# Kernel tuning notes

Hardware: AMD Instinct MI355X
Metric: run time of the kernel (lower is better)

The kernel has to match this reference:

```python
import jax, jax.numpy as jnp
import numpy as np

B, N, NSAMPLE = 8, 2048, 32
D = 64          # input feature channels
C1, C2 = 64, 128  # MLP channels (channels list after +3 on input: 67 -> 64 -> 128)
RADIUS = 0.15
EPS = 1e-5


def setup_inputs() -> dict:
    key = jax.random.key(0)
    ks = jax.random.split(key, 4)
    position = jax.random.uniform(ks[0], (B, N, 3), dtype=jnp.float32)
    feature = jax.random.normal(ks[1], (B, N, D), dtype=jnp.float32)
    W1 = jax.random.normal(ks[2], (D + 3, C1), dtype=jnp.float32) * 0.05
    gamma1 = jnp.ones((C1,), jnp.float32)
    beta1 = jnp.zeros((C1,), jnp.float32)
    W2 = jax.random.normal(ks[3], (C1, C2), dtype=jnp.float32) * 0.05
    gamma2 = jnp.ones((C2,), jnp.float32)
    beta2 = jnp.zeros((C2,), jnp.float32)
    return {"position": position, "feature": feature,
            "W1": W1, "gamma1": gamma1, "beta1": beta1,
            "W2": W2, "gamma2": gamma2, "beta2": beta2}


def _ball_query(xyz, radius, nsample):
    # squared pairwise distances [B, N, N]
    sq = (jnp.sum(xyz ** 2, -1)[:, :, None]
          + jnp.sum(xyz ** 2, -1)[:, None, :]
          - 2.0 * jnp.einsum('bnc,bmc->bnm', xyz, xyz))
    n = xyz.shape[1]
    idx = jnp.where(sq > radius ** 2, n, jnp.arange(n, dtype=jnp.int32)[None, None, :])
    idx = jnp.sort(idx, axis=-1)[:, :, :nsample]            # [B, N, nsample]
    first = idx[:, :, :1]
    return jnp.where(idx == n, first, idx)                  # pad misses with first neighbor


def _gather(points, idx):
    # points [B, N, C], idx [B, S, K] -> [B, S, K, C]
    b, s, k = idx.shape
    flat = jnp.take_along_axis(points, idx.reshape(b, s * k, 1), axis=1)
    return flat.reshape(b, s, k, points.shape[-1])


def _bn_relu(x, gamma, beta, relu=True):
    # BatchNorm1d over channel dim (train-mode stats across B*N*S), per linearblock
    mean = jnp.mean(x, axis=(0, 1, 2), keepdims=True)
    var = jnp.var(x, axis=(0, 1, 2), keepdims=True)
    y = (x - mean) * jax.lax.rsqrt(var + EPS) * gamma + beta
    return jax.nn.relu(y) if relu else y


def reference(position, feature, W1, gamma1, beta1, W2, gamma2, beta2):
    b, n, _ = position.shape
    idx = _ball_query(position, RADIUS, NSAMPLE)            # [B, N, nsample]
    grouped_xyz = _gather(position, idx) - position[:, :, None, :]  # [B,N,ns,3]
    grouped_feat = _gather(feature, idx)                    # [B, N, ns, D]
    h = jnp.concatenate([grouped_xyz, grouped_feat], axis=-1)  # [B, N, ns, 3+D]
    h = _bn_relu(h @ W1, gamma1, beta1)                     # [B, N, ns, C1]
    h = _bn_relu(h @ W2, gamma2, beta2)                     # [B, N, ns, C2]
    new_feature = jnp.max(h, axis=2)                        # [B, N, C2]
    return position, new_feature
```

## Files before the change

kernel.cpp:

```cpp
#include <hip/hip_runtime.h>
#include <hip/hip_bf16.h>


#define BB 8
#define NN 2048
#define KK 32
#define DD 64
#define CC1 64
#define CC2 128
#define TOTROWS (BB*NN*KK)
#define SITES (BB*NN)
#define PSLICES 256
#define DBLOCKS 1024

typedef __bf16 bf16x8 __attribute__((ext_vector_type(8)));
typedef float  f32x4  __attribute__((ext_vector_type(4)));

__device__ __forceinline__ void lds_add(float* p, float v) {
  __hip_atomic_fetch_add(p, v, __ATOMIC_RELAXED, __HIP_MEMORY_SCOPE_WORKGROUP);
}

__global__ __launch_bounds__(1024, 1) void kQ_ball_scatter(
    const float* __restrict__ pos, int* __restrict__ idx,
    float* __restrict__ Pc, float* __restrict__ Px,
    float* __restrict__ Py, float* __restrict__ Pz,
    float* __restrict__ momP)
{
  __shared__ float4 P[NN];
  __shared__ unsigned int Sc[NN], Sx[NN], Sy[NN], Sz[NN];
  __shared__ int idxL[64*KK];
  __shared__ float mred[16*9];
  const int b = blockIdx.x >> 5;
  const int slice = blockIdx.x & 31;
  for (int i = threadIdx.x; i < NN; i += 1024) {
    const float* p = pos + ((size_t)b*NN + i)*3;
    float x = p[0], y = p[1], z = p[2];
    float s = __fadd_rn(__fadd_rn(__fmul_rn(x,x), __fmul_rn(y,y)), __fmul_rn(z,z));
    P[i] = make_float4(x, y, z, s);
    Sc[i] = 0u; Sx[i] = 0u; Sy[i] = 0u; Sz[i] = 0u;
  }
  __syncthreads();
  const int wave = threadIdx.x >> 6, lane = threadIdx.x & 63;
  const float R2 = (float)(0.15 * 0.15);
  const unsigned long long lt = (lane == 63) ? 0x7fffffffffffffffull
                                             : ((1ull << lane) - 1ull);
  for (int qi = wave; qi < 64; qi += 16) {
    const int q = slice*64 + qi;
    const float4 Q = P[q];
    int* ip = idx + ((size_t)b*NN + q)*KK;
    int* il = idxL + qi*KK;
    int cnt = 0, first = -1;
    for (int step = 0; step < 32; ++step) {
      float4 p = P[step*64 + lane];
      float d = __fmul_rn(Q.x, p.x);
      d = fmaf(Q.y, p.y, d);
      d = fmaf(Q.z, p.z, d);
      float sq = __fsub_rn(__fadd_rn(Q.w, p.w), __fmul_rn(2.0f, d));
      bool in = !(sq > R2);
      unsigned long long mask = __ballot(in);
      if (first < 0 && mask) first = step*64 + (int)__builtin_ctzll(mask);
      int dst = cnt + (int)__popcll(mask & lt);
      if (in && dst < KK) { ip[dst] = step*64 + lane; il[dst] = step*64 + lane; }
      cnt += (int)__popcll(mask);
      if (cnt >= KK) break;
    }
    if (lane >= cnt && lane < KK) { ip[lane] = first; il[lane] = first; }
  }
  __syncthreads();
  const int sl = threadIdx.x >> 4;
  const int kg = threadIdx.x & 15;
  const int ip0 = idxL[sl*KK];
  const float4 C = P[slice*64 + sl];
  const float FS = 4194304.0f;
  float m1x=0.f,m1y=0.f,m1z=0.f,mxx=0.f,myy=0.f,mzz=0.f,mxy=0.f,mxz=0.f,myz=0.f;
  int wt = 0;
  #pragma unroll
  for (int j = 0; j < 2; ++j) {
    const int k = kg*2 + j;
    const int m = idxL[sl*KK + k];
    const float4 Pm = P[m];
    float dx = Pm.x - C.x;
    float dy = Pm.y - C.y;
    float dz = Pm.z - C.z;
    if (k > 0 && m == ip0) {
      ++wt;
    } else {
      atomicAdd(&Sc[m], 1u);
      atomicAdd(&Sx[m], (unsigned int)__float2int_rn(dx*FS));
      atomicAdd(&Sy[m], (unsigned int)__float2int_rn(dy*FS));
      atomicAdd(&Sz[m], (unsigned int)__float2int_rn(dz*FS));
    }
    m1x += dx; m1y += dy; m1z += dz;
    mxx = fmaf(dx,dx,mxx); myy = fmaf(dy,dy,myy); mzz = fmaf(dz,dz,mzz);
    mxy = fmaf(dx,dy,mxy); mxz = fmaf(dx,dz,mxz); myz = fmaf(dy,dz,myz);
  }
  if (wt > 0) {
    const float4 P0 = P[ip0];
    float dx0 = P0.x - C.x;
    float dy0 = P0.y - C.y;
    float dz0 = P0.z - C.z;
    atomicAdd(&Sc[ip0], (unsigned int)wt);
    atomicAdd(&Sx[ip0], (unsigned int)(wt*__float2int_rn(dx0*FS)));
    atomicAdd(&Sy[ip0], (unsigned int)(wt*__float2int_rn(dy0*FS)));
    atomicAdd(&Sz[ip0], (unsigned int)(wt*__float2int_rn(dz0*FS)));
  }
  const int wv = threadIdx.x >> 6;
  float vals[9] = {m1x,m1y,m1z,mxx,myy,mzz,mxy,mxz,myz};
  #pragma unroll
  for (int i = 0; i < 9; ++i) {
    float v = vals[i];
    #pragma unroll
    for (int s = 1; s < 64; s <<= 1) v += __shfl_xor(v, s, 64);
    if (lane == 0) mred[wv*9 + i] = v;
  }
  __syncthreads();
  const float IS = 2.38418579101562500e-7f;
  float* pc = Pc + (size_t)blockIdx.x*NN;
  float* px = Px + (size_t)blockIdx.x*NN;
  float* py = Py + (size_t)blockIdx.x*NN;
  float* pz = Pz + (size_t)blockIdx.x*NN;
  for (int i = threadIdx.x; i < NN; i += 1024) {
    pc[i] = (float)Sc[i];
    px[i] = (float)(int)Sx[i] * IS;
    py[i] = (float)(int)Sy[i] * IS;
    pz[i] = (float)(int)Sz[i] * IS;
  }
  if (threadIdx.x < 9) {
    float s = 0.f;
    #pragma unroll
    for (int w2 = 0; w2 < 16; ++w2) s += mred[w2*9 + threadIdx.x];
    momP[(size_t)blockIdx.x*16 + threadIdx.x] = s;
  }
}

__global__ __launch_bounds__(256) void kB_g(const float* __restrict__ feat,
                                            const float* __restrict__ W1,
                                            const float* __restrict__ Pc,
                                            const float* __restrict__ Px,
                                            const float* __restrict__ Py,
                                            const float* __restrict__ Pz,
                                            float* __restrict__ g,
                                            float* __restrict__ A_p)
{
  __shared__ float red[320];
  __shared__ float cntL[128], dxL[128], dyL[128], dzL[128];
  for (int i = threadIdx.x; i < 320; i += 256) red[i] = 0.f;
  const int row0B = blockIdx.x * 128;
  const int bb = row0B >> 11;
  for (int r2 = threadIdx.x; r2 < 128; r2 += 256) {
    const int m = (row0B + r2) & (NN-1);
    float s0 = 0.f, s1 = 0.f, s2 = 0.f, s3 = 0.f;
    #pragma unroll 4
    for (int q = 0; q < 32; ++q) {
      const size_t base = (size_t)(bb*32 + q)*NN + m;
      s0 += Pc[base]; s1 += Px[base]; s2 += Py[base]; s3 += Pz[base];
    }
    cntL[r2] = s0; dxL[r2] = s1; dyL[r2] = s2; dzL[r2] = s3;
  }
  __syncthreads();
  const int lane = threadIdx.x & 63;
  const int quad = lane >> 4;
  const int col  = lane & 15;
  const int gw = (blockIdx.x*256 + threadIdx.x) >> 6;

  bf16x8 Bf[2][4];
  #pragma unroll
  for (int kt = 0; kt < 2; ++kt)
    #pragma unroll
    for (int nt = 0; nt < 4; ++nt) {
      bf16x8 v;
      #pragma unroll
      for (int j = 0; j < 8; ++j)
        v[j] = (__bf16)W1[(3 + kt*32 + quad*8 + j)*CC1 + nt*16 + col];
      Bf[kt][nt] = v;
    }
  float a1[4], a2[4], a3[4], a4[4], a5[4];
  #pragma unroll
  for (int nt = 0; nt < 4; ++nt) { a1[nt]=0.f; a2[nt]=0.f; a3[nt]=0.f; a4[nt]=0.f; a5[nt]=0.f; }

  for (int t = 0; t < 2; ++t) {
    const int row0 = (gw*2 + t) * 16;
    bf16x8 Af[2];
    #pragma unroll
    for (int kt = 0; kt < 2; ++kt) {
      const float4* fp =
        (const float4*)(feat + (size_t)(row0 + col)*DD + kt*32 + quad*8);
      float4 f0 = fp[0], f1 = fp[1];
      float fv[8] = {f0.x,f0.y,f0.z,f0.w,f1.x,f1.y,f1.z,f1.w};
      bf16x8 v;
      #pragma unroll
      for (int j = 0; j < 8; ++j) v[j] = (__bf16)fv[j];
      Af[kt] = v;
    }
    float cw[4], dxw[4], dyw[4], dzw[4];
    #pragma unroll
    for (int r = 0; r < 4; ++r) {
      int rl = row0 - row0B + quad*4 + r;
      cw[r] = cntL[rl]; dxw[r] = dxL[rl]; dyw[r] = dyL[rl]; dzw[r] = dzL[rl];
    }
    #pragma unroll
    for (int nt = 0; nt < 4; ++nt) {
      f32x4 a = {0.f, 0.f, 0.f, 0.f};
      a = __builtin_amdgcn_mfma_f32_16x16x32_bf16(Af[0], Bf[0][nt], a, 0, 0, 0);
      a = __builtin_amdgcn_mfma_f32_16x16x32_bf16(Af[1], Bf[1][nt], a, 0, 0, 0);
      #pragma unroll
      for (int r = 0; r < 4; ++r) {
        float v = a[r];
        g[(size_t)(row0 + quad*4 + r)*CC1 + nt*16 + col] = v;
        float cv = cw[r]*v;
        a1[nt] += cv; a2[nt] = fmaf(cv, v, a2[nt]);
        a3[nt] = fmaf(dxw[r], v, a3[nt]);
        a4[nt] = fmaf(dyw[r], v, a4[nt]);
        a5[nt] = fmaf(dzw[r], v, a5[nt]);
      }
    }
  }
  #pragma unroll
  for (int nt = 0; nt < 4; ++nt) {
    float v1=a1[nt], v2=a2[nt], v3=a3[nt], v4=a4[nt], v5=a5[nt];
    v1 += __shfl_xor(v1,16,64); v1 += __shfl_xor(v1,32,64);
    v2 += __shfl_xor(v2,16,64); v2 += __shfl_xor(v2,32,64);
    v3 += __shfl_xor(v3,16,64); v3 += __shfl_xor(v3,32,64);
    v4 += __shfl_xor(v4,16,64); v4 += __shfl_xor(v4,32,64);
    v5 += __shfl_xor(v5,16,64); v5 += __shfl_xor(v5,32,64);
    if (quad == 0) {
      int ch = nt*16 + col;
      lds_add(&red[ch], v1);
      lds_add(&red[64+ch], v2);
      lds_add(&red[128+ch], v3);
      lds_add(&red[192+ch], v4);
      lds_add(&red[256+ch], v5);
    }
  }
  __syncthreads();
  for (int i = threadIdx.x; i < 320; i += 256)
    A_p[(size_t)blockIdx.x*320 + i] = red[i];
}

__global__ __launch_bounds__(256) void kS_fold(
    const float* __restrict__ W1, const float* __restrict__ gamma1,
    const float* __restrict__ beta1, const float* __restrict__ A_p,
    const float* __restrict__ momP,
    float* __restrict__ sc1, float* __restrict__ sh1, float* __restrict__ W1s)
{
  __shared__ float AL[320];
  __shared__ float mr[256];
  __shared__ float momL[16];
  {
    const int t = threadIdx.x;
    const int i = t & 15, jq = t >> 4;
    float s = 0.f;
    #pragma unroll
    for (int q = 0; q < 16; ++q) s += momP[(size_t)(jq*16 + q)*16 + i];
    mr[t] = s;
  }
  for (int c = threadIdx.x; c < 320; c += 256) {
    float s = 0.f;
    for (int blk = 0; blk < 128; ++blk) s += A_p[(size_t)blk*320 + c];
    AL[c] = s;
  }
  __syncthreads();
  if (threadIdx.x < 16) {
    float tot = 0.f;
    #pragma unroll
    for (int q = 0; q < 16; ++q) tot += mr[q*16 + threadIdx.x];
    momL[threadIdx.x] = tot;
  }
  __syncthreads();
  const int c = threadIdx.x;
  if (c >= CC1) return;
  float wx = W1[c], wy = W1[CC1+c], wz = W1[2*CC1+c];
  float A1 = AL[c], A2 = AL[64+c];
  float A3x = AL[128+c], A3y = AL[192+c], A3z = AL[256+c];
  float sum1 = A1 + wx*momL[0] + wy*momL[1] + wz*momL[2];
  float ss = A2 + 2.f*(wx*A3x + wy*A3y + wz*A3z)
           + wx*wx*momL[3] + wy*wy*momL[4] + wz*wz*momL[5]
           + 2.f*(wx*wy*momL[6] + wx*wz*momL[7] + wy*wz*momL[8]);
  const float invN = 1.0f / (float)TOTROWS;
  float mean = sum1 * invN;
  float var  = ss * invN - mean*mean;
  float sc = rsqrtf(var + 1e-5f) * gamma1[c];
  float sh = beta1[c] - mean * sc;
  sc1[c] = sc; sh1[c] = sh;
  W1s[c] = wx*sc; W1s[64+c] = wy*sc; W1s[128+c] = wz*sc;
}

__global__ __launch_bounds__(256, 2) void kD_mfma(
    const float* __restrict__ pos, const int* __restrict__ idx,
    const float* __restrict__ g, const float* __restrict__ sc1,
    const float* __restrict__ sh1, const float* __restrict__ W1s,
    const float* __restrict__ W2,
    float* __restrict__ stats2P, float* __restrict__ out_nf)
{
  __shared__ __bf16 W2T[CC2*72];
  __shared__ float red2[256];
  red2[threadIdx.x] = 0.f;
  {
    const int n  = threadIdx.x & 127;
    const int k0 = (threadIdx.x >> 7) << 5;
    #pragma unroll
    for (int jj = 0; jj < 4; ++jj) {
      unsigned int pk[4];
      #pragma unroll
      for (int q2 = 0; q2 < 4; ++q2) {
        const int k = k0 + jj*8 + q2*2;
        __bf16 lo = (__bf16)W2[(size_t)k*CC2 + n];
        __bf16 hi = (__bf16)W2[(size_t)(k+1)*CC2 + n];
        unsigned short ulo, uhi;
        __builtin_memcpy(&ulo, &lo, 2);
        __builtin_memcpy(&uhi, &hi, 2);
        pk[q2] = ((unsigned int)uhi << 16) | (unsigned int)ulo;
      }
      __builtin_memcpy(&W2T[n*72 + k0 + jj*8], pk, 16);
    }
  }
  __syncthreads();

  const int lane = threadIdx.x & 63;
  const int quad = lane >> 4;
  const int col  = lane & 15;
  const int wv = (blockIdx.x*256 + threadIdx.x) >> 6;

  float ssum[8], ssq[8];
  #pragma unroll
  for (int nt = 0; nt < 8; ++nt) { ssum[nt] = 0.f; ssq[nt] = 0.f; }

  #pragma clang loop unroll(disable)
  for (int si = 0; si < 4; ++si) {
    const int site = wv*4 + si;
    const int b  = site >> 11;
    const int ls = site & (NN-1);
    const float* pb = pos + (size_t)b*NN*3;
    const int* ip = idx + (size_t)site*KK;

    const int ma = ip[col], mb = ip[16 + col];
    const float ccx = pb[ls*3], ccy = pb[ls*3+1], ccz = pb[ls*3+2];
    const float dxa = pb[ma*3]-ccx, dya = pb[ma*3+1]-ccy, dza = pb[ma*3+2]-ccz;
    const float dxb = pb[mb*3]-ccx, dyb = pb[mb*3+1]-ccy, dzb = pb[mb*3+2]-ccz;

    const float* gbase = g + (size_t)b*NN*CC1;
    const float* ra = gbase + (size_t)ma*CC1 + quad*8;
    const float* rb = gbase + (size_t)mb*CC1 + quad*8;
    f32x4 gA0 = *(const f32x4*)ra,      gA1 = *(const f32x4*)(ra+4);
    f32x4 gA2 = *(const f32x4*)(ra+32), gA3 = *(const f32x4*)(ra+36);
    f32x4 gB0 = *(const f32x4*)rb,      gB1 = *(const f32x4*)(rb+4);
    f32x4 gB2 = *(const f32x4*)(rb+32), gB3 = *(const f32x4*)(rb+36);

    bf16x8 A00, A01, A10, A11;
    {
      const int c0 = quad*8;
      f32x4 x0 = *(const f32x4*)&W1s[c0],     x1 = *(const f32x4*)&W1s[c0+4];
      f32x4 y0 = *(const f32x4*)&W1s[64+c0],  y1 = *(const f32x4*)&W1s[64+c0+4];
      f32x4 z0 = *(const f32x4*)&W1s[128+c0], z1 = *(const f32x4*)&W1s[128+c0+4];
      f32x4 s0 = *(const f32x4*)&sc1[c0],     s1 = *(const f32x4*)&sc1[c0+4];
      f32x4 h0 = *(const f32x4*)&sh1[c0],     h1 = *(const f32x4*)&sh1[c0+4];
      #pragma unroll
      for (int j = 0; j < 8; ++j) {
        float wx = (j<4)?x0[j]:x1[j-4], wy = (j<4)?y0[j]:y1[j-4];
        float wz = (j<4)?z0[j]:z1[j-4], sc = (j<4)?s0[j]:s1[j-4];
        float sh = (j<4)?h0[j]:h1[j-4];
        float ga = (j<4)?gA0[j]:gA1[j-4], gb = (j<4)?gB0[j]:gB1[j-4];
        float ta = fmaf(dza, wz, fmaf(dya, wy, fmaf(dxa, wx, sh)));
        A00[j] = (__bf16)fmaxf(fmaf(ga, sc, ta), 0.f);
        float tb = fmaf(dzb, wz, fmaf(dyb, wy, fmaf(dxb, wx, sh)));
        A10[j] = (__bf16)fmaxf(fmaf(gb, sc, tb), 0.f);
      }
    }
    {
      const int c0 = 32 + quad*8;
      f32x4 x0 = *(const f32x4*)&W1s[c0],     x1 = *(const f32x4*)&W1s[c0+4];
      f32x4 y0 = *(const f32x4*)&W1s[64+c0],  y1 = *(const f32x4*)&W1s[64+c0+4];
      f32x4 z0 = *(const f32x4*)&W1s[128+c0], z1 = *(const f32x4*)&W1s[128+c0+4];
      f32x4 s0 = *(const f32x4*)&sc1[c0],     s1 = *(const f32x4*)&sc1[c0+4];
      f32x4 h0 = *(const f32x4*)&sh1[c0],     h1 = *(const f32x4*)&sh1[c0+4];
      #pragma unroll
      for (int j = 0; j < 8; ++j) {
        float wx = (j<4)?x0[j]:x1[j-4], wy = (j<4)?y0[j]:y1[j-4];
        float wz = (j<4)?z0[j]:z1[j-4], sc = (j<4)?s0[j]:s1[j-4];
        float sh = (j<4)?h0[j]:h1[j-4];
        float ga = (j<4)?gA2[j]:gA3[j-4], gb = (j<4)?gB2[j]:gB3[j-4];
        float ta = fmaf(dza, wz, fmaf(dya, wy, fmaf(dxa, wx, sh)));
        A01[j] = (__bf16)fmaxf(fmaf(ga, sc, ta), 0.f);
        float tb = fmaf(dzb, wz, fmaf(dyb, wy, fmaf(dxb, wx, sh)));
        A11[j] = (__bf16)fmaxf(fmaf(gb, sc, tb), 0.f);
      }
    }

    float* outp = out_nf + (size_t)site*CC2;
    #pragma unroll
    for (int nt = 0; nt < 8; ++nt) {
      const bf16x8 B0 = *(const bf16x8*)&W2T[(nt*16 + col)*72 + quad*8];
      const bf16x8 B1 = *(const bf16x8*)&W2T[(nt*16 + col)*72 + 32 + quad*8];
      float mxv = -3.0e38f;
      f32x4 a = {0.f, 0.f, 0.f, 0.f};
      a = __builtin_amdgcn_mfma_f32_16x16x32_bf16(A00, B0, a, 0, 0, 0);
      a = __builtin_amdgcn_mfma_f32_16x16x32_bf16(A01, B1, a, 0, 0, 0);
      #pragma unroll
      for (int r = 0; r < 4; ++r) {
        float v = a[r];
        ssum[nt] += v; ssq[nt] = fmaf(v, v, ssq[nt]); mxv = fmaxf(mxv, v);
      }
      f32x4 a2 = {0.f, 0.f, 0.f, 0.f};
      a2 = __builtin_amdgcn_mfma_f32_16x16x32_bf16(A10, B0, a2, 0, 0, 0);
      a2 = __builtin_amdgcn_mfma_f32_16x16x32_bf16(A11, B1, a2, 0, 0, 0);
      #pragma unroll
      for (int r = 0; r < 4; ++r) {
        float v = a2[r];
        ssum[nt] += v; ssq[nt] = fmaf(v, v, ssq[nt]); mxv = fmaxf(mxv, v);
      }
      mxv = fmaxf(mxv, __shfl_xor(mxv, 16, 64));
      mxv = fmaxf(mxv, __shfl_xor(mxv, 32, 64));
      if ((nt & 3) == quad) outp[nt*16 + col] = mxv;
    }
  }

  #pragma unroll
  for (int nt = 0; nt < 8; ++nt) {
    float s = ssum[nt];
    s += __shfl_xor(s, 16, 64); s += __shfl_xor(s, 32, 64);
    float q = ssq[nt];
    q += __shfl_xor(q, 16, 64); q += __shfl_xor(q, 32, 64);
    if (lane < 16) {
      atomicAdd(&red2[nt*16 + col], s);
      atomicAdd(&red2[128 + nt*16 + col], q);
    }
  }
  __syncthreads();
  stats2P[(size_t)blockIdx.x*256 + threadIdx.x] = red2[threadIdx.x];
}

__global__ __launch_bounds__(256) void kR2_stats(
    const float* __restrict__ stats2P, float* __restrict__ stats2)
{
  __shared__ float r[256];
  const int c = blockIdx.x;
  float s = 0.f;
  for (int i = threadIdx.x; i < DBLOCKS; i += 256)
    s += stats2P[(size_t)i*256 + c];
  r[threadIdx.x] = s;
  __syncthreads();
  for (int off = 128; off > 0; off >>= 1) {
    if (threadIdx.x < off) r[threadIdx.x] += r[threadIdx.x + off];
    __syncthreads();
  }
  if (threadIdx.x == 0) stats2[c] = r[0];
}

__global__ __launch_bounds__(256) void k45_epi(const float* __restrict__ pos,
                                               const float* __restrict__ g2,
                                               const float* __restrict__ be2,
                                               const float* __restrict__ stats2,
                                               float* __restrict__ out)
{
  int i = blockIdx.x*256 + threadIdx.x;
  if (blockIdx.x < 192) { out[i] = pos[i]; return; }
  int j = i - 192*256;
  int c = j & (CC2-1);
  const float invc = 1.0f / (float)TOTROWS;
  float mean = stats2[c] * invc;
  float var  = stats2[128 + c] * invc - mean*mean;
  float sc = rsqrtf(var + 1e-5f) * g2[c];
  float sh = be2[c] - mean * sc;
  float* out_nf = out + (size_t)BB*NN*3;
  float x = out_nf[j];
  out_nf[j] = fmaxf(fmaf(x, sc, sh), 0.f);
}

extern "C" void kernel_launch(void* const* d_in, const int* in_sizes, int n_in,
                              void* d_out, int out_size, void* d_ws, size_t ws_size,
                              hipStream_t stream) {
  const float* pos  = (const float*)d_in[0];
  const float* feat = (const float*)d_in[1];
  const float* W1   = (const float*)d_in[2];
  const float* g1   = (const float*)d_in[3];
  const float* be1  = (const float*)d_in[4];
  const float* W2   = (const float*)d_in[5];
  const float* g2   = (const float*)d_in[6];
  const float* be2  = (const float*)d_in[7];
  float* out = (float*)d_out;
  float* out_nf = out + (size_t)BB*NN*3;

  char* w = (char*)d_ws;
  int*   idx    = (int*)w;
  float* stats2 = (float*)(w + 0x200000);
  float* sc1    = stats2 + 256;
  float* sh1    = sc1 + 64;
  float* W1s    = sh1 + 64;
  float* A_p    = (float*)(w + 0x210000);
  float* momP   = (float*)(w + 0x250000);
  float* Pc     = (float*)(w + 0x260000);
  float* Px     = Pc + (size_t)PSLICES*NN;
  float* Py     = Px + (size_t)PSLICES*NN;
  float* Pz     = Py + (size_t)PSLICES*NN;
  float* stats2P= (float*)(w + 0x660000);
  float* g      = (float*)(w + 0xA60000);

  kQ_ball_scatter<<<256, 1024, 0, stream>>>(pos, idx, Pc, Px, Py, Pz, momP);
  kB_g      <<<128, 256, 0, stream>>>(feat, W1, Pc, Px, Py, Pz, g, A_p);
  kS_fold   <<<1, 256, 0, stream>>>(W1, g1, be1, A_p, momP, sc1, sh1, W1s);
  kD_mfma   <<<DBLOCKS, 256, 0, stream>>>(pos, idx, g, sc1, sh1, W1s, W2,
                                          stats2P, out_nf);
  kR2_stats <<<256, 256, 0, stream>>>(stats2P, stats2);
  k45_epi   <<<192 + (SITES*CC2)/256, 256, 0, stream>>>(pos, g2, be2, stats2, out);
}
```

Before: 173.6 us.

## Fuse all stages into one cooperative persistent kernel with grid syncs

Replaces the six kernel launches with one cooperative kernel of 256 blocks by 1024 threads, which uses grid.sync between the ball-query/scatter, layer-1 stats, layer-2 MFMA and epilogue stages. Neighbor indices now stay in LDS instead of being written to and re-read from global memory. This removes launch gaps and the idx round trip. The cost is that later stages run with fewer, larger blocks and each block serially reduces the per-block partials, and the large LDS footprint holds occupancy to one block per CU.

After: 370.7 us. 114% more time.

```diff
diff --git a/kernel.cpp b/kernel.cpp
--- a/kernel.cpp
+++ b/kernel.cpp
@@ -1,5 +1,8 @@
 #include <hip/hip_runtime.h>
 #include <hip/hip_bf16.h>
+#include <hip/hip_cooperative_groups.h>
+
+namespace cg = cooperative_groups;
 
 
 #define BB 8
@@ -10,8 +13,7 @@
 #define CC2 128
 #define TOTROWS (BB*NN*KK)
 #define SITES (BB*NN)
-#define PSLICES 256
-#define DBLOCKS 1024
+#define NBLK 256
 
 typedef __bf16 bf16x8 __attribute__((ext_vector_type(8)));
 typedef float  f32x4  __attribute__((ext_vector_type(4)));
@@ -20,450 +22,417 @@
   __hip_atomic_fetch_add(p, v, __ATOMIC_RELAXED, __HIP_MEMORY_SCOPE_WORKGROUP);
 }
 
-__global__ __launch_bounds__(1024, 1) void kQ_ball_scatter(
-    const float* __restrict__ pos, int* __restrict__ idx,
+__global__ __launch_bounds__(1024, 1) void kMega(
+    const float* __restrict__ pos, const float* __restrict__ feat,
+    const float* __restrict__ W1, const float* __restrict__ gamma1,
+    const float* __restrict__ beta1, const float* __restrict__ W2,
+    const float* __restrict__ gamma2, const float* __restrict__ beta2,
+    float* __restrict__ out,
     float* __restrict__ Pc, float* __restrict__ Px,
     float* __restrict__ Py, float* __restrict__ Pz,
-    float* __restrict__ momP)
+    float* __restrict__ momP, float* __restrict__ gbuf,
+    float* __restrict__ A_p, float* __restrict__ stats2P)
 {
   __shared__ float4 P[NN];
+  __shared__ int idxL[64*KK];
   __shared__ unsigned int Sc[NN], Sx[NN], Sy[NN], Sz[NN];
-  __shared__ int idxL[64*KK];
   __shared__ float mred[16*9];
-  const int b = blockIdx.x >> 5;
-  const int slice = blockIdx.x & 31;
-  for (int i = threadIdx.x; i < NN; i += 1024) {
-    const float* p = pos + ((size_t)b*NN + i)*3;
-    float x = p[0], y = p[1], z = p[2];
+  __shared__ float redB[320];
+  __shared__ float cntL[64], dxLs[64], dyLs[64], dzLs[64];
+  __shared__ alignas(16) float AL[320];
+  __shared__ float momL[16];
+  __shared__ alignas(16) float sc1L[64];
+  __shared__ alignas(16) float sh1L[64];
+  __shared__ alignas(16) float W1sL[192];
+  __shared__ alignas(16) __bf16 W2T[CC2*72];
+  __shared__ float red2[256];
+  __shared__ float stF[256];
+  __shared__ float scL[128], shL[128];
+
+  cg::grid_group grid = cg::this_grid();
+
+  const int p = blockIdx.x;
+  const int b = p >> 5;
+  const int slice = p & 31;
+  const int t = threadIdx.x;
+  const int wave = t >> 6, lane = t & 63;
+  const int quad = lane >> 4;
+  const int col  = lane & 15;
+  float* out_nf = out + (size_t)BB*NN*3;
+
+  for (int i = t; i < NN; i += 1024) {
+    const float* pp = pos + ((size_t)b*NN + i)*3;
+    float x = pp[0], y = pp[1], z = pp[2];
     float s = __fadd_rn(__fadd_rn(__fmul_rn(x,x), __fmul_rn(y,y)), __fmul_rn(z,z));
     P[i] = make_float4(x, y, z, s);
     Sc[i] = 0u; Sx[i] = 0u; Sy[i] = 0u; Sz[i] = 0u;
   }
   __syncthreads();
-  const int wave = threadIdx.x >> 6, lane = threadIdx.x & 63;
-  const float R2 = (float)(0.15 * 0.15);
-  const unsigned long long lt = (lane == 63) ? 0x7fffffffffffffffull
-                                             : ((1ull << lane) - 1ull);
-  for (int qi = wave; qi < 64; qi += 16) {
-    const int q = slice*64 + qi;
-    const float4 Q = P[q];
-    int* ip = idx + ((size_t)b*NN + q)*KK;
-    int* il = idxL + qi*KK;
-    int cnt = 0, first = -1;
-    for (int step = 0; step < 32; ++step) {
-      float4 p = P[step*64 + lane];
-      float d = __fmul_rn(Q.x, p.x);
-      d = fmaf(Q.y, p.y, d);
-      d = fmaf(Q.z, p.z, d);
-      float sq = __fsub_rn(__fadd_rn(Q.w, p.w), __fmul_rn(2.0f, d));
-      bool in = !(sq > R2);
-      unsigned long long mask = __ballot(in);
-      if (first < 0 && mask) first = step*64 + (int)__builtin_ctzll(mask);
-      int dst = cnt + (int)__popcll(mask & lt);
-      if (in && dst < KK) { ip[dst] = step*64 + lane; il[dst] = step*64 + lane; }
-      cnt += (int)__popcll(mask);
-      if (cnt >= KK) break;
-    }
-    if (lane >= cnt && lane < KK) { ip[lane] = first; il[lane] = first; }
-  }
-  __syncthreads();
-  const int sl = threadIdx.x >> 4;
-  const int kg = threadIdx.x & 15;
-  const int ip0 = idxL[sl*KK];
-  const float4 C = P[slice*64 + sl];
-  const float FS = 4194304.0f;
-  float m1x=0.f,m1y=0.f,m1z=0.f,mxx=0.f,myy=0.f,mzz=0.f,mxy=0.f,mxz=0.f,myz=0.f;
-  int wt = 0;
-  #pragma unroll
-  for (int j = 0; j < 2; ++j) {
-    const int k = kg*2 + j;
-    const int m = idxL[sl*KK + k];
-    const float4 Pm = P[m];
-    float dx = Pm.x - C.x;
-    float dy = Pm.y - C.y;
-    float dz = Pm.z - C.z;
-    if (k > 0 && m == ip0) {
-      ++wt;
-    } else {
-      atomicAdd(&Sc[m], 1u);
-      atomicAdd(&Sx[m], (unsigned int)__float2int_rn(dx*FS));
-      atomicAdd(&Sy[m], (unsigned int)__float2int_rn(dy*FS));
-      atomicAdd(&Sz[m], (unsigned int)__float2int_rn(dz*FS));
-    }
-    m1x += dx; m1y += dy; m1z += dz;
-    mxx = fmaf(dx,dx,mxx); myy = fmaf(dy,dy,myy); mzz = fmaf(dz,dz,mzz);
-    mxy = fmaf(dx,dy,mxy); mxz = fmaf(dx,dz,mxz); myz = fmaf(dy,dz,myz);
-  }
-  if (wt > 0) {
-    const float4 P0 = P[ip0];
-    float dx0 = P0.x - C.x;
-    float dy0 = P0.y - C.y;
-    float dz0 = P0.z - C.z;
-    atomicAdd(&Sc[ip0], (unsigned int)wt);
-    atomicAdd(&Sx[ip0], (unsigned int)(wt*__float2int_rn(dx0*FS)));
-    atomicAdd(&Sy[ip0], (unsigned int)(wt*__float2int_rn(dy0*FS)));
-    atomicAdd(&Sz[ip0], (unsigned int)(wt*__float2int_rn(dz0*FS)));
-  }
-  const int wv = threadIdx.x >> 6;
-  float vals[9] = {m1x,m1y,m1z,mxx,myy,mzz,mxy,mxz,myz};
-  #pragma unroll
-  for (int i = 0; i < 9; ++i) {
-    float v = vals[i];
+  {
+    const float R2 = (float)(0.15 * 0.15);
+    const unsigned long long lt = (lane == 63) ? 0x7fffffffffffffffull
+                                               : ((1ull << lane) - 1ull);
+    for (int qi = wave; qi < 64; qi += 16) {
+      const int q = slice*64 + qi;
+      const float4 Q = P[q];
+      int* il = idxL + qi*KK;
+      int cnt = 0, first = -1;
+      for (int step = 0; step < 32; ++step) {
+        float4 pp = P[step*64 + lane];
+        float d = __fmul_rn(Q.x, pp.x);
+        d = fmaf(Q.y, pp.y, d);
+        d = fmaf(Q.z, pp.z, d);
+        float sq = __fsub_rn(__fadd_rn(Q.w, pp.w), __fmul_rn(2.0f, d));
+        bool in = !(sq > R2);
+        unsigned long long mask = __ballot(in);
+        if (first < 0 && mask) first = step*64 + (int)__builtin_ctzll(mask);
+        int dst = cnt + (int)__popcll(mask & lt);
+        if (in && dst < KK) il[dst] = step*64 + lane;
+        cnt += (int)__popcll(mask);
+        if (cnt >= KK) break;
+      }
+      if (lane >= cnt && lane < KK) il[lane] = first;
+    }
+  }
+  __syncthreads();
+  {
+    const int sl = t >> 4;
+    const int kg = t & 15;
+    const int ip0 = idxL[sl*KK];
+    const float4 C = P[slice*64 + sl];
+    const float FS = 4194304.0f;
+    float m1x=0.f,m1y=0.f,m1z=0.f,mxx=0.f,myy=0.f,mzz=0.f,mxy=0.f,mxz=0.f,myz=0.f;
+    int wt = 0;
     #pragma unroll
-    for (int s = 1; s < 64; s <<= 1) v += __shfl_xor(v, s, 64);
-    if (lane == 0) mred[wv*9 + i] = v;
-  }
-  __syncthreads();
-  const float IS = 2.38418579101562500e-7f;
-  float* pc = Pc + (size_t)blockIdx.x*NN;
-  float* px = Px + (size_t)blockIdx.x*NN;
-  float* py = Py + (size_t)blockIdx.x*NN;
-  float* pz = Pz + (size_t)blockIdx.x*NN;
-  for (int i = threadIdx.x; i < NN; i += 1024) {
-    pc[i] = (float)Sc[i];
-    px[i] = (float)(int)Sx[i] * IS;
-    py[i] = (float)(int)Sy[i] * IS;
-    pz[i] = (float)(int)Sz[i] * IS;
-  }
-  if (threadIdx.x < 9) {
-    float s = 0.f;
+    for (int j = 0; j < 2; ++j) {
+      const int k = kg*2 + j;
+      const int m = idxL[sl*KK + k];
+      const float4 Pm = P[m];
+      float dx = Pm.x - C.x;
+      float dy = Pm.y - C.y;
+      float dz = Pm.z - C.z;
+      if (k > 0 && m == ip0) {
+        ++wt;
+      } else {
+        atomicAdd(&Sc[m], 1u);
+        atomicAdd(&Sx[m], (unsigned int)__float2int_rn(dx*FS));
+        atomicAdd(&Sy[m], (unsigned int)__float2int_rn(dy*FS));
+        atomicAdd(&Sz[m], (unsigned int)__float2int_rn(dz*FS));
+      }
+      m1x += dx; m1y += dy; m1z += dz;
+      mxx = fmaf(dx,dx,mxx); myy = fmaf(dy,dy,myy); mzz = fmaf(dz,dz,mzz);
+      mxy = fmaf(dx,dy,mxy); mxz = fmaf(dx,dz,mxz); myz = fmaf(dy,dz,myz);
+    }
+    if (wt > 0) {
+      const float4 P0 = P[ip0];
+      float dx0 = P0.x - C.x;
+      float dy0 = P0.y - C.y;
+      float dz0 = P0.z - C.z;
+      atomicAdd(&Sc[ip0], (unsigned int)wt);
+      atomicAdd(&Sx[ip0], (unsigned int)(wt*__float2int_rn(dx0*FS)));
+      atomicAdd(&Sy[ip0], (unsigned int)(wt*__float2int_rn(dy0*FS)));
+      atomicAdd(&Sz[ip0], (unsigned int)(wt*__float2int_rn(dz0*FS)));
+    }
+    float vals[9] = {m1x,m1y,m1z,mxx,myy,mzz,mxy,mxz,myz};
     #pragma unroll
-    for (int w2 = 0; w2 < 16; ++w2) s += mred[w2*9 + threadIdx.x];
-    momP[(size_t)blockIdx.x*16 + threadIdx.x] = s;
-  }
-}
-
-__global__ __launch_bounds__(256) void kB_g(const float* __restrict__ feat,
-                                            const float* __restrict__ W1,
-                                            const float* __restrict__ Pc,
-                                            const float* __restrict__ Px,
-                                            const float* __restrict__ Py,
-                                            const float* __restrict__ Pz,
-                                            float* __restrict__ g,
-                                            float* __restrict__ A_p)
-{
-  __shared__ float red[320];
-  __shared__ float cntL[128], dxL[128], dyL[128], dzL[128];
-  for (int i = threadIdx.x; i < 320; i += 256) red[i] = 0.f;
-  const int row0B = blockIdx.x * 128;
-  const int bb = row0B >> 11;
-  for (int r2 = threadIdx.x; r2 < 128; r2 += 256) {
-    const int m = (row0B + r2) & (NN-1);
-    float s0 = 0.f, s1 = 0.f, s2 = 0.f, s3 = 0.f;
-    #pragma unroll 4
-    for (int q = 0; q < 32; ++q) {
-      const size_t base = (size_t)(bb*32 + q)*NN + m;
-      s0 += Pc[base]; s1 += Px[base]; s2 += Py[base]; s3 += Pz[base];
-    }
-    cntL[r2] = s0; dxL[r2] = s1; dyL[r2] = s2; dzL[r2] = s3;
-  }
-  __syncthreads();
-  const int lane = threadIdx.x & 63;
-  const int quad = lane >> 4;
-  const int col  = lane & 15;
-  const int gw = (blockIdx.x*256 + threadIdx.x) >> 6;
-
-  bf16x8 Bf[2][4];
-  #pragma unroll
-  for (int kt = 0; kt < 2; ++kt)
+    for (int i = 0; i < 9; ++i) {
+      float v = vals[i];
+      #pragma unroll
+      for (int s = 1; s < 64; s <<= 1) v += __shfl_xor(v, s, 64);
+      if (lane == 0) mred[wave*9 + i] = v;
+    }
+  }
+  __syncthreads();
+  {
+    const float IS = 2.38418579101562500e-7f;
+    float* pc = Pc + (size_t)p*NN;
+    float* px = Px + (size_t)p*NN;
+    float* py = Py + (size_t)p*NN;
+    float* pz = Pz + (size_t)p*NN;
+    for (int i = t; i < NN; i += 1024) {
+      pc[i] = (float)Sc[i];
+      px[i] = (float)(int)Sx[i] * IS;
+      py[i] = (float)(int)Sy[i] * IS;
+      pz[i] = (float)(int)Sz[i] * IS;
+    }
+    if (t < 9) {
+      float s = 0.f;
+      #pragma unroll
+      for (int w2 = 0; w2 < 16; ++w2) s += mred[w2*9 + t];
+      momP[(size_t)p*16 + t] = s;
+    }
+  }
+
+  grid.sync();
+
+  {
+    const int row0B = p * 64;
+    if (t < 64) {
+      const int m = (row0B + t) & (NN-1);
+      float s0 = 0.f, s1 = 0.f, s2 = 0.f, s3 = 0.f;
+      #pragma unroll 4
+      for (int q = 0; q < 32; ++q) {
+        const size_t base = (size_t)(b*32 + q)*NN + m;
+        s0 += Pc[base]; s1 += Px[base]; s2 += Py[base]; s3 += Pz[base];
+      }
+      cntL[t] = s0; dxLs[t] = s1; dyLs[t] = s2; dzLs[t] = s3;
+    }
+    if (t < 320) redB[t] = 0.f;
+    __syncthreads();
+    if (wave < 4) {
+      const int row0 = row0B + wave*16;
+      bf16x8 Bf[2][4];
+      #pragma unroll
+      for (int kt = 0; kt < 2; ++kt)
+        #pragma unroll
+        for (int nt = 0; nt < 4; ++nt) {
+          bf16x8 v;
+          #pragma unroll
+          for (int j = 0; j < 8; ++j)
+            v[j] = (__bf16)W1[(3 + kt*32 + quad*8 + j)*CC1 + nt*16 + col];
+          Bf[kt][nt] = v;
+        }
+      bf16x8 Af[2];
+      #pragma unroll
+      for (int kt = 0; kt < 2; ++kt) {
+        const float4* fp =
+          (const float4*)(feat + (size_t)(row0 + col)*DD + kt*32 + quad*8);
+        float4 f0 = fp[0], f1 = fp[1];
+        float fv[8] = {f0.x,f0.y,f0.z,f0.w,f1.x,f1.y,f1.z,f1.w};
+        bf16x8 v;
+        #pragma unroll
+        for (int j = 0; j < 8; ++j) v[j] = (__bf16)fv[j];
+        Af[kt] = v;
+      }
+      float cw[4], dxw[4], dyw[4], dzw[4];
+      #pragma unroll
+      for (int r = 0; r < 4; ++r) {
+        int rl = wave*16 + quad*4 + r;
+        cw[r] = cntL[rl]; dxw[r] = dxLs[rl]; dyw[r] = dyLs[rl]; dzw[r] = dzLs[rl];
+      }
+      float a1[4], a2[4], a3[4], a4[4], a5[4];
+      #pragma unroll
+      for (int nt = 0; nt < 4; ++nt) { a1[nt]=0.f; a2[nt]=0.f; a3[nt]=0.f; a4[nt]=0.f; a5[nt]=0.f; }
+      #pragma unroll
+      for (int nt = 0; nt < 4; ++nt) {
+        f32x4 a = {0.f, 0.f, 0.f, 0.f};
+        a = __builtin_amdgcn_mfma_f32_16x16x32_bf16(Af[0], Bf[0][nt], a, 0, 0, 0);
+        a = __builtin_amdgcn_mfma_f32_16x16x32_bf16(Af[1], Bf[1][nt], a, 0, 0, 0);
+        #pragma unroll
+        for (int r = 0; r < 4; ++r) {
+          float v = a[r];
+          gbuf[(size_t)(row0 + quad*4 + r)*CC1 + nt*16 + col] = v;
+          float cv = cw[r]*v;
+          a1[nt] += cv; a2[nt] = fmaf(cv, v, a2[nt]);
+          a3[nt] = fmaf(dxw[r], v, a3[nt]);
+          a4[nt] = fmaf(dyw[r], v, a4[nt]);
+          a5[nt] = fmaf(dzw[r], v, a5[nt]);
+        }
+      }
+      #pragma unroll
+      for (int nt = 0; nt < 4; ++nt) {
+        float v1=a1[nt], v2=a2[nt], v3=a3[nt], v4=a4[nt], v5=a5[nt];
+        v1 += __shfl_xor(v1,16,64); v1 += __shfl_xor(v1,32,64);
+        v2 += __shfl_xor(v2,16,64); v2 += __shfl_xor(v2,32,64);
+        v3 += __shfl_xor(v3,16,64); v3 += __shfl_xor(v3,32,64);
+        v4 += __shfl_xor(v4,16,64); v4 += __shfl_xor(v4,32,64);
+        v5 += __shfl_xor(v5,16,64); v5 += __shfl_xor(v5,32,64);
+        if (quad == 0) {
+          int ch = nt*16 + col;
+          lds_add(&redB[ch], v1);
+          lds_add(&redB[64+ch], v2);
+          lds_add(&redB[128+ch], v3);
+          lds_add(&redB[192+ch], v4);
+          lds_add(&redB[256+ch], v5);
+        }
+      }
+    }
+    __syncthreads();
+    if (t < 320) A_p[(size_t)p*320 + t] = redB[t];
+  }
+
+  grid.sync();
+
+  {
+    const int n  = t & 127;
+    const int kq = t >> 7;
+    unsigned int pk[4];
     #pragma unroll
-    for (int nt = 0; nt < 4; ++nt) {
-      bf16x8 v;
-      #pragma unroll
-      for (int j = 0; j < 8; ++j)
-        v[j] = (__bf16)W1[(3 + kt*32 + quad*8 + j)*CC1 + nt*16 + col];
-      Bf[kt][nt] = v;
-    }
-  float a1[4], a2[4], a3[4], a4[4], a5[4];
-  #pragma unroll
-  for (int nt = 0; nt < 4; ++nt) { a1[nt]=0.f; a2[nt]=0.f; a3[nt]=0.f; a4[nt]=0.f; a5[nt]=0.f; }
-
-  for (int t = 0; t < 2; ++t) {
-    const int row0 = (gw*2 + t) * 16;
-    bf16x8 Af[2];
+    for (int q2 = 0; q2 < 4; ++q2) {
+      const int k = kq*8 + q2*2;
+      __bf16 lo = (__bf16)W2[(size_t)k*CC2 + n];
+      __bf16 hi = (__bf16)W2[(size_t)(k+1)*CC2 + n];
+      unsigned short ulo, uhi;
+      __builtin_memcpy(&ulo, &lo, 2);
+      __builtin_memcpy(&uhi, &hi, 2);
+      pk[q2] = ((unsigned int)uhi << 16) | (unsigned int)ulo;
+    }
+    __builtin_memcpy(&W2T[n*72 + kq*8], pk, 16);
+    if (t < 256) red2[t] = 0.f;
+    if (t < 320) {
+      float s = 0.f;
+      for (int blk = 0; blk < NBLK; ++blk) s += A_p[(size_t)blk*320 + t];
+      AL[t] = s;
+    }
+    if (t < 16) {
+      float s = 0.f;
+      for (int blk = 0; blk < NBLK; ++blk) s += momP[(size_t)blk*16 + t];
+      momL[t] = s;
+    }
+  }
+  __syncthreads();
+  if (t < CC1) {
+    const int c = t;
+    float wx = W1[c], wy = W1[CC1+c], wz = W1[2*CC1+c];
+    float A1 = AL[c], A2 = AL[64+c];
+    float A3x = AL[128+c], A3y = AL[192+c], A3z = AL[256+c];
+    float sum1 = A1 + wx*momL[0] + wy*momL[1] + wz*momL[2];
+    float ss = A2 + 2.f*(wx*A3x + wy*A3y + wz*A3z)
+             + wx*wx*momL[3] + wy*wy*momL[4] + wz*wz*momL[5]
+             + 2.f*(wx*wy*momL[6] + wx*wz*momL[7] + wy*wz*momL[8]);
+    const float invN = 1.0f / (float)TOTROWS;
+    float mean = sum1 * invN;
+    float var  = ss * invN - mean*mean;
+    float sc = rsqrtf(var + 1e-5f) * gamma1[c];
+    float sh = beta1[c] - mean * sc;
+    sc1L[c] = sc; sh1L[c] = sh;
+    W1sL[c] = wx*sc; W1sL[64+c] = wy*sc; W1sL[128+c] = wz*sc;
+  }
+  __syncthreads();
+
+  {
+    float ssum[8], ssq[8];
     #pragma unroll
-    for (int kt = 0; kt < 2; ++kt) {
-      const float4* fp =
-        (const float4*)(feat + (size_t)(row0 + col)*DD + kt*32 + quad*8);
-      float4 f0 = fp[0], f1 = fp[1];
-      float fv[8] = {f0.x,f0.y,f0.z,f0.w,f1.x,f1.y,f1.z,f1.w};
-      bf16x8 v;
-      #pragma unroll
-      for (int j = 0; j < 8; ++j) v[j] = (__bf16)fv[j];
-      Af[kt] = v;
-    }
-    float cw[4], dxw[4], dyw[4], dzw[4];
-    #pragma unroll
-    for (int r = 0; r < 4; ++r) {
-      int rl = row0 - row0B + quad*4 + r;
-      cw[r] = cntL[rl]; dxw[r] = dxL[rl]; dyw[r] = dyL[rl]; dzw[r] = dzL[rl];
-    }
-    #pragma unroll
-    for (int nt = 0; nt < 4; ++nt) {
-      f32x4 a = {0.f, 0.f, 0.f, 0.f};
-      a = __builtin_amdgcn_mfma_f32_16x16x32_bf16(Af[0], Bf[0][nt], a, 0, 0, 0);
-      a = __builtin_amdgcn_mfma_f32_16x16x32_bf16(Af[1], Bf[1][nt], a, 0, 0, 0);
-      #pragma unroll
-      for (int r = 0; r < 4; ++r) {
-        float v = a[r];
-        g[(size_t)(row0 + quad*4 + r)*CC1 + nt*16 + col] = v;
-        float cv = cw[r]*v;
-        a1[nt] += cv; a2[nt] = fmaf(cv, v, a2[nt]);
-        a3[nt] = fmaf(dxw[r], v, a3[nt]);
-        a4[nt] = fmaf(dyw[r], v, a4[nt]);
-        a5[nt] = fmaf(dzw[r], v, a5[nt]);
-      }
-    }
-  }
-  #pragma unroll
-  for (int nt = 0; nt < 4; ++nt) {
-    float v1=a1[nt], v2=a2[nt], v3=a3[nt], v4=a4[nt], v5=a5[nt];
-    v1 += __shfl_xor(v1,16,64); v1 += __shfl_xor(v1,32,64);
-    v2 += __shfl_xor(v2,16,64); v2 += __shfl_xor(v2,32,64);
-    v3 += __shfl_xor(v3,16,64); v3 += __shfl_xor(v3,32,64);
-    v4 += __shfl_xor(v4,16,64); v4 += __shfl_xor(v4,32,64);
-    v5 += __shfl_xor(v5,16,64); v5 += __shfl_xor(v5,32,64);
-    if (quad == 0) {
-      int ch = nt*16 + col;
-      lds_add(&red[ch], v1);
-      lds_add(&red[64+ch], v2);
-      lds_add(&red[128+ch], v3);
-      lds_add(&red[192+ch], v4);
-      lds_add(&red[256+ch], v5);
-    }
-  }
-  __syncthreads();
-  for (int i = threadIdx.x; i < 320; i += 256)
-    A_p[(size_t)blockIdx.x*320 + i] = red[i];
-}
-
-__global__ __launch_bounds__(256) void kS_fold(
-    const float* __restrict__ W1, const float* __restrict__ gamma1,
-    const float* __restrict__ beta1, const float* __restrict__ A_p,
-    const float* __restrict__ momP,
-    float* __restrict__ sc1, float* __restrict__ sh1, float* __restrict__ W1s)
-{
-  __shared__ float AL[320];
-  __shared__ float mr[256];
-  __shared__ float momL[16];
-  {
-    const int t = threadIdx.x;
-    const int i = t & 15, jq = t >> 4;
-    float s = 0.f;
-    #pragma unroll
-    for (int q = 0; q < 16; ++q) s += momP[(size_t)(jq*16 + q)*16 + i];
-    mr[t] = s;
-  }
-  for (int c = threadIdx.x; c < 320; c += 256) {
-    float s = 0.f;
-    for (int blk = 0; blk < 128; ++blk) s += A_p[(size_t)blk*320 + c];
-    AL[c] = s;
-  }
-  __syncthreads();
-  if (threadIdx.x < 16) {
-    float tot = 0.f;
-    #pragma unroll
-    for (int q = 0; q < 16; ++q) tot += mr[q*16 + threadIdx.x];
-    momL[threadIdx.x] = tot;
-  }
-  __syncthreads();
-  const int c = threadIdx.x;
-  if (c >= CC1) return;
-  float wx = W1[c], wy = W1[CC1+c], wz = W1[2*CC1+c];
-  float A1 = AL[c], A2 = AL[64+c];
-  float A3x = AL[128+c], A3y = AL[192+c], A3z = AL[256+c];
-  float sum1 = A1 + wx*momL[0] + wy*momL[1] + wz*momL[2];
-  float ss = A2 + 2.f*(wx*A3x + wy*A3y + wz*A3z)
-           + wx*wx*momL[3] + wy*wy*momL[4] + wz*wz*momL[5]
-           + 2.f*(wx*wy*momL[6] + wx*wz*momL[7] + wy*wz*momL[8]);
-  const float invN = 1.0f / (float)TOTROWS;
-  float mean = sum1 * invN;
-  float var  = ss * invN - mean*mean;
-  float sc = rsqrtf(var + 1e-5f) * gamma1[c];
-  float sh = beta1[c] - mean * sc;
-  sc1[c] = sc; sh1[c] = sh;
-  W1s[c] = wx*sc; W1s[64+c] = wy*sc; W1s[128+c] = wz*sc;
-}
-
-__global__ __launch_bounds__(256, 2) void kD_mfma(
-    const float* __restrict__ pos, const int* __restrict__ idx,
-    const float* __restrict__ g, const float* __restrict__ sc1,
-    const float* __restrict__ sh1, const float* __restrict__ W1s,
-    const float* __restrict__ W2,
-    float* __restrict__ stats2P, float* __restrict__ out_nf)
-{
-  __shared__ __bf16 W2T[CC2*72];
-  __shared__ float red2[256];
-  red2[threadIdx.x] = 0.f;
-  {
-    const int n  = threadIdx.x & 127;
-    const int k0 = (threadIdx.x >> 7) << 5;
-    #pragma unroll
-    for (int jj = 0; jj < 4; ++jj) {
-      unsigned int pk[4];
-      #pragma unroll
-      for (int q2 = 0; q2 < 4; ++q2) {
-        const int k = k0 + jj*8 + q2*2;
-        __bf16 lo = (__bf16)W2[(size_t)k*CC2 + n];
-        __bf16 hi = (__bf16)W2[(size_t)(k+1)*CC2 + n];
-        unsigned short ulo, uhi;
-        __builtin_memcpy(&ulo, &lo, 2);
-        __builtin_memcpy(&uhi, &hi, 2);
-        pk[q2] = ((unsigned int)uhi << 16) | (unsigned int)ulo;
-      }
-      __builtin_memcpy(&W2T[n*72 + k0 + jj*8], pk, 16);
-    }
-  }
-  __syncthreads();
-
-  const int lane = threadIdx.x & 63;
-  const int quad = lane >> 4;
-  const int col  = lane & 15;
-  const int wv = (blockIdx.x*256 + threadIdx.x) >> 6;
-
-  float ssum[8], ssq[8];
-  #pragma unroll
-  for (int nt = 0; nt < 8; ++nt) { ssum[nt] = 0.f; ssq[nt] = 0.f; }
-
-  #pragma clang loop unroll(disable)
-  for (int si = 0; si < 4; ++si) {
-    const int site = wv*4 + si;
-    const int b  = site >> 11;
-    const int ls = site & (NN-1);
-    const float* pb = pos + (size_t)b*NN*3;
-    const int* ip = idx + (size_t)site*KK;
-
-    const int ma = ip[col], mb = ip[16 + col];
-    const float ccx = pb[ls*3], ccy = pb[ls*3+1], ccz = pb[ls*3+2];
-    const float dxa = pb[ma*3]-ccx, dya = pb[ma*3+1]-ccy, dza = pb[ma*3+2]-ccz;
-    const float dxb = pb[mb*3]-ccx, dyb = pb[mb*3+1]-ccy, dzb = pb[mb*3+2]-ccz;
-
-    const float* gbase = g + (size_t)b*NN*CC1;
-    const float* ra = gbase + (size_t)ma*CC1 + quad*8;
-    const float* rb = gbase + (size_t)mb*CC1 + quad*8;
-    f32x4 gA0 = *(const f32x4*)ra,      gA1 = *(const f32x4*)(ra+4);
-    f32x4 gA2 = *(const f32x4*)(ra+32), gA3 = *(const f32x4*)(ra+36);
-    f32x4 gB0 = *(const f32x4*)rb,      gB1 = *(const f32x4*)(rb+4);
-    f32x4 gB2 = *(const f32x4*)(rb+32), gB3 = *(const f32x4*)(rb+36);
-
-    bf16x8 A00, A01, A10, A11;
-    {
-      const int c0 = quad*8;
-      f32x4 x0 = *(const f32x4*)&W1s[c0],     x1 = *(const f32x4*)&W1s[c0+4];
-      f32x4 y0 = *(const f32x4*)&W1s[64+c0],  y1 = *(const f32x4*)&W1s[64+c0+4];
-      f32x4 z0 = *(const f32x4*)&W1s[128+c0], z1 = *(const f32x4*)&W1s[128+c0+4];
-      f32x4 s0 = *(const f32x4*)&sc1[c0],     s1 = *(const f32x4*)&sc1[c0+4];
-      f32x4 h0 = *(const f32x4*)&sh1[c0],     h1 = *(const f32x4*)&sh1[c0+4];
-      #pragma unroll
-      for (int j = 0; j < 8; ++j) {
-        float wx = (j<4)?x0[j]:x1[j-4], wy = (j<4)?y0[j]:y1[j-4];
-        float wz = (j<4)?z0[j]:z1[j-4], sc = (j<4)?s0[j]:s1[j-4];
-        float sh = (j<4)?h0[j]:h1[j-4];
-        float ga = (j<4)?gA0[j]:gA1[j-4], gb = (j<4)?gB0[j]:gB1[j-4];
-        float ta = fmaf(dza, wz, fmaf(dya, wy, fmaf(dxa, wx, sh)));
-        A00[j] = (__bf16)fmaxf(fmaf(ga, sc, ta), 0.f);
-        float tb = fmaf(dzb, wz, fmaf(dyb, wy, fmaf(dxb, wx, sh)));
-        A10[j] = (__bf16)fmaxf(fmaf(gb, sc, tb), 0.f);
-      }
-    }
-    {
-      const int c0 = 32 + quad*8;
-      f32x4 x0 = *(const f32x4*)&W1s[c0],     x1 = *(const f32x4*)&W1s[c0+4];
-      f32x4 y0 = *(const f32x4*)&W1s[64+c0],  y1 = *(const f32x4*)&W1s[64+c0+4];
-      f32x4 z0 = *(const f32x4*)&W1s[128+c0], z1 = *(const f32x4*)&W1s[128+c0+4];
-      f32x4 s0 = *(const f32x4*)&sc1[c0],     s1 = *(const f32x4*)&sc1[c0+4];
-      f32x4 h0 = *(const f32x4*)&sh1[c0],     h1 = *(const f32x4*)&sh1[c0+4];
-      #pragma unroll
-      for (int j = 0; j < 8; ++j) {
-        float wx = (j<4)?x0[j]:x1[j-4], wy = (j<4)?y0[j]:y1[j-4];
-        float wz = (j<4)?z0[j]:z1[j-4], sc = (j<4)?s0[j]:s1[j-4];
-        float sh = (j<4)?h0[j]:h1[j-4];
-        float ga = (j<4)?gA2[j]:gA3[j-4], gb = (j<4)?gB2[j]:gB3[j-4];
-        float ta = fmaf(dza, wz, fmaf(dya, wy, fmaf(dxa, wx, sh)));
-        A01[j] = (__bf16)fmaxf(fmaf(ga, sc, ta), 0.f);
-        float tb = fmaf(dzb, wz, fmaf(dyb, wy, fmaf(dxb, wx, sh)));
-        A11[j] = (__bf16)fmaxf(fmaf(gb, sc, tb), 0.f);
-      }
-    }
-
-    float* outp = out_nf + (size_t)site*CC2;
+    for (int nt = 0; nt < 8; ++nt) { ssum[nt] = 0.f; ssq[nt] = 0.f; }
+    const float* gbase = gbuf + (size_t)b*NN*CC1;
+
+    #pragma clang loop unroll(disable)
+    for (int si = 0; si < 4; ++si) {
+      const int sl4 = wave*4 + si;
+      const int siteg = p*64 + sl4;
+      const int ma = idxL[sl4*KK + col], mb = idxL[sl4*KK + 16 + col];
+      const float4 C = P[slice*64 + sl4];
+      const float4 Pa = P[ma], Pb = P[mb];
+      const float dxa = Pa.x-C.x, dya = Pa.y-C.y, dza = Pa.z-C.z;
+      const float dxb = Pb.x-C.x, dyb = Pb.y-C.y, dzb = Pb.z-C.z;
+
+      const float* ra = gbase + (size_t)ma*CC1 + quad*8;
+      const float* rb = gbase + (size_t)mb*CC1 + quad*8;
+      f32x4 gA0 = *(const f32x4*)ra,      gA1 = *(const f32x4*)(ra+4);
+      f32x4 gA2 = *(const f32x4*)(ra+32), gA3 = *(const f32x4*)(ra+36);
+      f32x4 gB0 = *(const f32x4*)rb,      gB1 = *(const f32x4*)(rb+4);
+      f32x4 gB2 = *(const f32x4*)(rb+32), gB3 = *(const f32x4*)(rb+36);
+
+      bf16x8 A00, A01, A10, A11;
+      {
+        const int c0 = quad*8;
+        f32x4 x0 = *(const f32x4*)&W1sL[c0],     x1 = *(const f32x4*)&W1sL[c0+4];
+        f32x4 y0 = *(const f32x4*)&W1sL[64+c0],  y1 = *(const f32x4*)&W1sL[64+c0+4];
+        f32x4 z0 = *(const f32x4*)&W1sL[128+c0], z1 = *(const f32x4*)&W1sL[128+c0+4];
+        f32x4 s0 = *(const f32x4*)&sc1L[c0],     s1 = *(const f32x4*)&sc1L[c0+4];
+        f32x4 h0 = *(const f32x4*)&sh1L[c0],     h1 = *(const f32x4*)&sh1L[c0+4];
+        #pragma unroll
+        for (int j = 0; j < 8; ++j) {
+          float wx = (j<4)?x0[j]:x1[j-4], wy = (j<4)?y0[j]:y1[j-4];
+          float wz = (j<4)?z0[j]:z1[j-4], sc = (j<4)?s0[j]:s1[j-4];
+          float sh = (j<4)?h0[j]:h1[j-4];
+          float ga = (j<4)?gA0[j]:gA1[j-4], gb = (j<4)?gB0[j]:gB1[j-4];
+          float ta = fmaf(dza, wz, fmaf(dya, wy, fmaf(dxa, wx, sh)));
+          A00[j] = (__bf16)fmaxf(fmaf(ga, sc, ta), 0.f);
+          float tb = fmaf(dzb, wz, fmaf(dyb, wy, fmaf(dxb, wx, sh)));
+          A10[j] = (__bf16)fmaxf(fmaf(gb, sc, tb), 0.f);
+        }
+      }
+      {
+        const int c0 = 32 + quad*8;
+        f32x4 x0 = *(const f32x4*)&W1sL[c0],     x1 = *(const f32x4*)&W1sL[c0+4];
+        f32x4 y0 = *(const f32x4*)&W1sL[64+c0],  y1 = *(const f32x4*)&W1sL[64+c0+4];
+        f32x4 z0 = *(const f32x4*)&W1sL[128+c0], z1 = *(const f32x4*)&W1sL[128+c0+4];
+        f32x4 s0 = *(const f32x4*)&sc1L[c0],     s1 = *(const f32x4*)&sc1L[c0+4];
+        f32x4 h0 = *(const f32x4*)&sh1L[c0],     h1 = *(const f32x4*)&sh1L[c0+4];
+        #pragma unroll
+        for (int j = 0; j < 8; ++j) {
+          float wx = (j<4)?x0[j]:x1[j-4], wy = (j<4)?y0[j]:y1[j-4];
+          float wz = (j<4)?z0[j]:z1[j-4], sc = (j<4)?s0[j]:s1[j-4];
+          float sh = (j<4)?h0[j]:h1[j-4];
+          float ga = (j<4)?gA2[j]:gA3[j-4], gb = (j<4)?gB2[j]:gB3[j-4];
+          float ta = fmaf(dza, wz, fmaf(dya, wy, fmaf(dxa, wx, sh)));
+          A01[j] = (__bf16)fmaxf(fmaf(ga, sc, ta), 0.f);
+          float tb = fmaf(dzb, wz, fmaf(dyb, wy, fmaf(dxb, wx, sh)));
+          A11[j] = (__bf16)fmaxf(fmaf(gb, sc, tb), 0.f);
+        }
+      }
+
+      float* outp = out_nf + (size_t)siteg*CC2;
+      #pragma unroll
+      for (int nt = 0; nt < 8; ++nt) {
+        const bf16x8 B0 = *(const bf16x8*)&W2T[(nt*16 + col)*72 + quad*8];
+        const bf16x8 B1 = *(const bf16x8*)&W2T[(nt*16 + col)*72 + 32 + quad*8];
+        float mxv = -3.0e38f;
+        f32x4 a = {0.f, 0.f, 0.f, 0.f};
+        a = __builtin_amdgcn_mfma_f32_16x16x32_bf16(A00, B0, a, 0, 0, 0);
+        a = __builtin_amdgcn_mfma_f32_16x16x32_bf16(A01, B1, a, 0, 0, 0);
+        #pragma unroll
+        for (int r = 0; r < 4; ++r) {
+          float v = a[r];
+          ssum[nt] += v; ssq[nt] = fmaf(v, v, ssq[nt]); mxv = fmaxf(mxv, v);
+        }
+        f32x4 a2 = {0.f, 0.f, 0.f, 0.f};
+        a2 = __builtin_amdgcn_mfma_f32_16x16x32_bf16(A10, B0, a2, 0, 0, 0);
+        a2 = __builtin_amdgcn_mfma_f32_16x16x32_bf16(A11, B1, a2, 0, 0, 0);
+        #pragma unroll
+        for (int r = 0; r < 4; ++r) {
+          float v = a2[r];
+          ssum[nt] += v; ssq[nt] = fmaf(v, v, ssq[nt]); mxv = fmaxf(mxv, v);
+        }
+        mxv = fmaxf(mxv, __shfl_xor(mxv, 16, 64));
+        mxv = fmaxf(mxv, __shfl_xor(mxv, 32, 64));
+        if ((nt & 3) == quad) outp[nt*16 + col] = mxv;
+      }
+    }
+
     #pragma unroll
     for (int nt = 0; nt < 8; ++nt) {
-      const bf16x8 B0 = *(const bf16x8*)&W2T[(nt*16 + col)*72 + quad*8];
-      const bf16x8 B1 = *(const bf16x8*)&W2T[(nt*16 + col)*72 + 32 + quad*8];
-      float mxv = -3.0e38f;
-      f32x4 a = {0.f, 0.f, 0.f, 0.f};
-      a = __builtin_amdgcn_mfma_f32_16x16x32_bf16(A00, B0, a, 0, 0, 0);
-      a = __builtin_amdgcn_mfma_f32_16x16x32_bf16(A01, B1, a, 0, 0, 0);
-      #pragma unroll
-      for (int r = 0; r < 4; ++r) {
-        float v = a[r];
-        ssum[nt] += v; ssq[nt] = fmaf(v, v, ssq[nt]); mxv = fmaxf(mxv, v);
-      }
-      f32x4 a2 = {0.f, 0.f, 0.f, 0.f};
-      a2 = __builtin_amdgcn_mfma_f32_16x16x32_bf16(A10, B0, a2, 0, 0, 0);
-      a2 = __builtin_amdgcn_mfma_f32_16x16x32_bf16(A11, B1, a2, 0, 0, 0);
-      #pragma unroll
-      for (int r = 0; r < 4; ++r) {
-        float v = a2[r];
-        ssum[nt] += v; ssq[nt] = fmaf(v, v, ssq[nt]); mxv = fmaxf(mxv, v);
-      }
-      mxv = fmaxf(mxv, __shfl_xor(mxv, 16, 64));
-      mxv = fmaxf(mxv, __shfl_xor(mxv, 32, 64));
-      if ((nt & 3) == quad) outp[nt*16 + col] = mxv;
-    }
-  }
-
-  #pragma unroll
-  for (int nt = 0; nt < 8; ++nt) {
-    float s = ssum[nt];
-    s += __shfl_xor(s, 16, 64); s += __shfl_xor(s, 32, 64);
-    float q = ssq[nt];
-    q += __shfl_xor(q, 16, 64); q += __shfl_xor(q, 32, 64);
-    if (lane < 16) {
-      atomicAdd(&red2[nt*16 + col], s);
-      atomicAdd(&red2[128 + nt*16 + col], q);
-    }
-  }
-  __syncthreads();
-  stats2P[(size_t)blockIdx.x*256 + threadIdx.x] = red2[threadIdx.x];
-}
-
-__global__ __launch_bounds__(256) void kR2_stats(
-    const float* __restrict__ stats2P, float* __restrict__ stats2)
-{
-  __shared__ float r[256];
-  const int c = blockIdx.x;
-  float s = 0.f;
-  for (int i = threadIdx.x; i < DBLOCKS; i += 256)
-    s += stats2P[(size_t)i*256 + c];
-  r[threadIdx.x] = s;
-  __syncthreads();
-  for (int off = 128; off > 0; off >>= 1) {
-    if (threadIdx.x < off) r[threadIdx.x] += r[threadIdx.x + off];
+      float s = ssum[nt];
+      s += __shfl_xor(s, 16, 64); s += __shfl_xor(s, 32, 64);
+      float q = ssq[nt];
+      q += __shfl_xor(q, 16, 64); q += __shfl_xor(q, 32, 64);
+      if (lane < 16) {
+        atomicAdd(&red2[nt*16 + col], s);
+        atomicAdd(&red2[128 + nt*16 + col], q);
+      }
+    }
     __syncthreads();
-  }
-  if (threadIdx.x == 0) stats2[c] = r[0];
-}
-
-__global__ __launch_bounds__(256) void k45_epi(const float* __restrict__ pos,
-                                               const float* __restrict__ g2,
-                                               const float* __restrict__ be2,
-                                               const float* __restrict__ stats2,
-                                               float* __restrict__ out)
-{
-  int i = blockIdx.x*256 + threadIdx.x;
-  if (blockIdx.x < 192) { out[i] = pos[i]; return; }
-  int j = i - 192*256;
-  int c = j & (CC2-1);
-  const float invc = 1.0f / (float)TOTROWS;
-  float mean = stats2[c] * invc;
-  float var  = stats2[128 + c] * invc - mean*mean;
-  float sc = rsqrtf(var + 1e-5f) * g2[c];
-  float sh = be2[c] - mean * sc;
-  float* out_nf = out + (size_t)BB*NN*3;
-  float x = out_nf[j];
-  out_nf[j] = fmaxf(fmaf(x, sc, sh), 0.f);
+    if (t < 256) stats2P[(size_t)p*256 + t] = red2[t];
+  }
+
+  grid.sync();
+
+  if (t < 192) out[p*192 + t] = pos[p*192 + t];
+  if (t < 256) {
+    float s = 0.f;
+    for (int blk = 0; blk < NBLK; ++blk) s += stats2P[(size_t)blk*256 + t];
+    stF[t] = s;
+  }
+  __syncthreads();
+  if (t < CC2) {
+    const float invc = 1.0f / (float)TOTROWS;
+    float mean = stF[t] * invc;
+    float var  = stF[128 + t] * invc - mean*mean;
+    float sc = rsqrtf(var + 1e-5f) * gamma2[t];
+    float sh = beta2[t] - mean * sc;
+    scL[t] = sc; shL[t] = sh;
+  }
+  __syncthreads();
+  {
+    const size_t j0 = (size_t)p * 8192;
+    for (int e = t; e < 8192; e += 1024) {
+      const size_t j = j0 + e;
+      const int c = (int)(j & (CC2-1));
+      float x = out_nf[j];
+      out_nf[j] = fmaxf(fmaf(x, scL[c], shL[c]), 0.f);
+    }
+  }
 }
 
 extern "C" void kernel_launch(void* const* d_in, const int* in_sizes, int n_in,
@@ -478,28 +447,23 @@
   const float* g2   = (const float*)d_in[6];
   const float* be2  = (const float*)d_in[7];
   float* out = (float*)d_out;
-  float* out_nf = out + (size_t)BB*NN*3;
 
   char* w = (char*)d_ws;
-  int*   idx    = (int*)w;
-  float* stats2 = (float*)(w + 0x200000);
-  float* sc1    = stats2 + 256;
-  float* sh1    = sc1 + 64;
-  float* W1s    = sh1 + 64;
-  float* A_p    = (float*)(w + 0x210000);
-  float* momP   = (float*)(w + 0x250000);
-  float* Pc     = (float*)(w + 0x260000);
-  float* Px     = Pc + (size_t)PSLICES*NN;
-  float* Py     = Px + (size_t)PSLICES*NN;
-  float* Pz     = Py + (size_t)PSLICES*NN;
-  float* stats2P= (float*)(w + 0x660000);
-  float* g      = (float*)(w + 0xA60000);
-
-  kQ_ball_scatter<<<256, 1024, 0, stream>>>(pos, idx, Pc, Px, Py, Pz, momP);
-  kB_g      <<<128, 256, 0, stream>>>(feat, W1, Pc, Px, Py, Pz, g, A_p);
-  kS_fold   <<<1, 256, 0, stream>>>(W1, g1, be1, A_p, momP, sc1, sh1, W1s);
-  kD_mfma   <<<DBLOCKS, 256, 0, stream>>>(pos, idx, g, sc1, sh1, W1s, W2,
-                                          stats2P, out_nf);
-  kR2_stats <<<256, 256, 0, stream>>>(stats2P, stats2);
-  k45_epi   <<<192 + (SITES*CC2)/256, 256, 0, stream>>>(pos, g2, be2, stats2, out);
+  float* Pc      = (float*)w;
+  float* Px      = Pc + (size_t)NBLK*NN;
+  float* Py      = Px + (size_t)NBLK*NN;
+  float* Pz      = Py + (size_t)NBLK*NN;
+  float* gbuf    = (float*)(w + 0x800000);
+  float* A_p     = (float*)(w + 0xC00000);
+  float* momP    = (float*)(w + 0xC60000);
+  float* stats2P = (float*)(w + 0xC70000);
+
+  void* args[] = {
+    (void*)&pos, (void*)&feat, (void*)&W1, (void*)&g1, (void*)&be1,
+    (void*)&W2, (void*)&g2, (void*)&be2, (void*)&out,
+    (void*)&Pc, (void*)&Px, (void*)&Py, (void*)&Pz,
+    (void*)&momP, (void*)&gbuf, (void*)&A_p, (void*)&stats2P
+  };
+  hipLaunchCooperativeKernel((const void*)kMega, dim3(NBLK), dim3(1024),
+                             args, 0, stream);
 }
```
